# Kernel optimization log

Measured on AMD Instinct MI355X. Metric: run time of the kernel, lower is better.

Reference implementation:

```python
import jax, jax.numpy as jnp
import numpy as np

DIM = 1024
HEADS = 16
HEAD_DIM = DIM // HEADS
SCALE = HEAD_DIM ** -0.5
HIDDEN = 4 * DIM
EPS = 1e-5


def _ln(x, g, b):
    m = jnp.mean(x, -1, keepdims=True)
    v = jnp.mean(jnp.square(x - m), -1, keepdims=True)
    return (x - m) / jnp.sqrt(v + EPS) * g + b


def _attn(x, wqkv, qb, vb, wp, bp):
    # x: (B, N, C). qkv bias = concat(q_bias, zeros, v_bias) as in the torch code.
    B, N, C = x.shape
    bias = jnp.concatenate([qb, jnp.zeros_like(vb), vb])
    qkv = (x @ wqkv.T + bias).reshape(B, N, 3, HEADS, HEAD_DIM).transpose(2, 0, 3, 1, 4)
    q, k, v = qkv[0], qkv[1], qkv[2]
    # qk_float=True: logits computed in float32
    logits = jnp.einsum('bhqd,bhkd->bhqk', (q * SCALE).astype(jnp.float32), k.astype(jnp.float32))
    a = jax.nn.softmax(logits, axis=-1).astype(x.dtype)
    o = jnp.einsum('bhqk,bhkd->bqhd', a, v).reshape(B, N, C)
    return o @ wp.T + bp


def setup_inputs() -> dict:
    key = jax.random.key(0)
    ks = jax.random.split(key, 16)
    s = 0.02
    d = {
        'x': jax.random.normal(ks[0], (4, 8, 196, DIM), jnp.float32),
        'cls_token': jax.random.normal(ks[1], (4, DIM), jnp.float32),
        # temporal branch
        'tln_g': jnp.ones((DIM,), jnp.float32), 'tln_b': jnp.zeros((DIM,), jnp.float32),
        't_wqkv': jax.random.normal(ks[2], (3 * DIM, DIM), jnp.float32) * s,
        't_qb': jax.random.normal(ks[3], (DIM,), jnp.float32) * s,
        't_vb': jax.random.normal(ks[4], (DIM,), jnp.float32) * s,
        't_wproj': jax.random.normal(ks[5], (DIM, DIM), jnp.float32) * s,
        't_bproj': jnp.zeros((DIM,), jnp.float32),
        't_fc_w': jax.random.normal(ks[6], (DIM, DIM), jnp.float32) * s,
        't_fc_b': jnp.zeros((DIM,), jnp.float32),
        # spatial branch
        'n1_g': jnp.ones((DIM,), jnp.float32), 'n1_b': jnp.zeros((DIM,), jnp.float32),
        's_wqkv': jax.random.normal(ks[7], (3 * DIM, DIM), jnp.float32) * s,
        's_qb': jax.random.normal(ks[8], (DIM,), jnp.float32) * s,
        's_vb': jax.random.normal(ks[9], (DIM,), jnp.float32) * s,
        's_wproj': jax.random.normal(ks[10], (DIM, DIM), jnp.float32) * s,
        's_bproj': jnp.zeros((DIM,), jnp.float32),
        # mlp
        'n2_g': jnp.ones((DIM,), jnp.float32), 'n2_b': jnp.zeros((DIM,), jnp.float32),
        'fc1_w': jax.random.normal(ks[11], (HIDDEN, DIM), jnp.float32) * s,
        'fc1_b': jnp.zeros((HIDDEN,), jnp.float32),
        'fc2_w': jax.random.normal(ks[12], (DIM, HIDDEN), jnp.float32) * s,
        'fc2_b': jnp.zeros((DIM,), jnp.float32),
    }
    return d


def reference(x, cls_token, tln_g, tln_b, t_wqkv, t_qb, t_vb, t_wproj, t_bproj,
              t_fc_w, t_fc_b, n1_g, n1_b, s_wqkv, s_qb, s_vb, s_wproj, s_bproj,
              n2_g, n2_b, fc1_w, fc1_b, fc2_w, fc2_b):
    B, T, N, C = x.shape
    # temporal attention: 'b t n m -> (b n) t m'
    xt = x.transpose(0, 2, 1, 3).reshape(B * N, T, C)
    xt = _attn(_ln(xt, tln_g, tln_b), t_wqkv, t_qb, t_vb, t_wproj, t_bproj)
    # '(b n) t m -> b (n t) m'
    xt = xt.reshape(B, N * T, C)
    xt = xt @ t_fc_w.T + t_fc_b
    xt = x.transpose(0, 2, 1, 3).reshape(B, N * T, C) + xt
    # spatial attention with cls token per frame
    init_cls = cls_token[:, None, :]                               # (B, 1, C)
    cls_rep = jnp.broadcast_to(init_cls, (B, T, C)).reshape(B * T, 1, C)
    xs = xt.reshape(B, N, T, C).transpose(0, 2, 1, 3).reshape(B * T, N, C)
    xs = jnp.concatenate([cls_rep, xs], axis=1)                    # (B*T, N+1, C)
    xs = _attn(_ln(xs, n1_g, n1_b), s_wqkv, s_qb, s_vb, s_wproj, s_bproj)
    cls_m = xs[:, 0, :].reshape(B, T, C).mean(axis=1, keepdims=True)  # (B, 1, C)
    xs = xs[:, 1:, :].reshape(B, T, N, C).transpose(0, 2, 1, 3).reshape(B, N * T, C)
    x2 = jnp.concatenate([init_cls, xt], axis=1) + jnp.concatenate([cls_m, xs], axis=1)
    # MLP (exact GELU, matching nn.GELU default)
    h = _ln(x2, n2_g, n2_b)
    h = jax.nn.gelu(h @ fc1_w.T + fc1_b, approximate=False) @ fc2_w.T + fc2_b
    x2 = x2 + h
    cls_out = x2[:, 0, :]
    xo = x2[:, 1:].reshape(B, N, T, C).transpose(0, 2, 1, 3)       # (B, T, N, C)
    return xo, cls_out
```

## Files before the change

kernel.cpp:

```cpp
#include <hip/hip_runtime.h>
#include <stdint.h>


#define SCALE 0.125f

typedef unsigned short u16;
typedef short bf16x8 __attribute__((ext_vector_type(8)));
typedef float f32x4 __attribute__((ext_vector_type(4)));

static constexpr int kNT    = 1568;
static constexpr int kRowsA = 6272;
static constexpr int kSeqS  = 197;
static constexpr int kRowsS = 6304;
static constexpr int kRowsC = 6276;
static constexpr size_t kXO = 6422528;

__device__ __forceinline__ float bf2f(u16 u) {
    union { unsigned int i; float f; } c; c.i = ((unsigned int)u) << 16; return c.f;
}
__device__ __forceinline__ u16 f2bf(float f) {
    union { float f; unsigned int i; } c; c.f = f;
    unsigned int r = c.i + 0x7FFFu + ((c.i >> 16) & 1u);
    return (u16)(r >> 16);
}

__device__ __forceinline__ void gll16(const void* g, void* l) {
    __builtin_amdgcn_global_load_lds((__attribute__((address_space(1))) void*)g,
                                     (__attribute__((address_space(3))) void*)l,
                                     16, 0, 0);
}

__global__ void convw_k(const float* __restrict__ in, u16* __restrict__ out, int n4) {
    const int stride = gridDim.x * blockDim.x;
    for (int i = blockIdx.x * blockDim.x + threadIdx.x; i < n4; i += stride) {
        float4 v = ((const float4*)in)[i];
        ushort4 o;
        o.x = f2bf(v.x); o.y = f2bf(v.y); o.z = f2bf(v.z); o.w = f2bf(v.w);
        ((ushort4*)out)[i] = o;
    }
}

__global__ void bias3_k(const float* __restrict__ qb, const float* __restrict__ vb,
                        float* __restrict__ dst) {
    const int i = blockIdx.x * 256 + threadIdx.x;
    if (i >= 3072) return;
    dst[i] = (i < 1024) ? qb[i] : (i < 2048) ? 0.0f : vb[i - 2048];
}

template<int MODE>
__global__ void ln_k(const float* __restrict__ src, const float* __restrict__ src2,
                     const float* __restrict__ g, const float* __restrict__ bt,
                     u16* __restrict__ out, int rows) {
    const int r = (blockIdx.x << 2) + (threadIdx.x >> 6);
    const int lane = threadIdx.x & 63;
    if (r >= rows) return;
    const float* srow;
    if constexpr (MODE == 0) {
        int b = r / kNT, rem = r - b * kNT, n = rem >> 3, t = rem & 7;
        srow = src + (((size_t)((b * 8 + t) * 196 + n)) << 10);
    } else if constexpr (MODE == 1) {
        int s2 = r / kSeqS, i = r - s2 * kSeqS, b = s2 >> 3, t = s2 & 7;
        srow = (i == 0) ? (src2 + ((size_t)b << 10))
                        : (src + (((size_t)(b * kNT + ((i - 1) << 3) + t)) << 10));
    } else {
        srow = src + ((size_t)r << 10);
    }
    float4 v[4]; float s = 0.f, ss = 0.f;
#pragma unroll
    for (int j = 0; j < 4; ++j) {
        v[j] = *(const float4*)&srow[((j << 6) + lane) << 2];
        s  += v[j].x + v[j].y + v[j].z + v[j].w;
        ss += v[j].x * v[j].x + v[j].y * v[j].y + v[j].z * v[j].z + v[j].w * v[j].w;
    }
#pragma unroll
    for (int off = 1; off < 64; off <<= 1) { s += __shfl_xor(s, off); ss += __shfl_xor(ss, off); }
    const float mean = s * (1.f / 1024.f);
    const float rstd = rsqrtf(ss * (1.f / 1024.f) - mean * mean + 1e-5f);
#pragma unroll
    for (int j = 0; j < 4; ++j) {
        const int c = ((j << 6) + lane) << 2;
        float4 gg = *(const float4*)&g[c];
        float4 bb = *(const float4*)&bt[c];
        ushort4 o;
        o.x = f2bf((v[j].x - mean) * rstd * gg.x + bb.x);
        o.y = f2bf((v[j].y - mean) * rstd * gg.y + bb.y);
        o.z = f2bf((v[j].z - mean) * rstd * gg.z + bb.z);
        o.w = f2bf((v[j].w - mean) * rstd * gg.w + bb.w);
        *(ushort4*)&out[((size_t)r << 10) + c] = o;
    }
}

template<int MODE>
__global__ __launch_bounds__(256, 2) void gemm_bt(
        const u16* __restrict__ A, const u16* __restrict__ W,
        const float* __restrict__ bias,
        u16* __restrict__ outB, float* __restrict__ outF,
        const float* __restrict__ resid, float* __restrict__ dout,
        int M, int N, int K) {
    __shared__ __align__(16) u16 As[2][8192];
    __shared__ __align__(16) u16 Bs[2][8192];
    const int tid  = threadIdx.x;
    const int lane = tid & 63, wave = tid >> 6;
    const int lo = lane & 15, hi = lane >> 4;
    const int wr = wave >> 1, wc = wave & 1;
    const int row0 = blockIdx.y << 7, col0 = blockIdx.x << 7;

    const u16* aP[4]; const u16* bP[4];
#pragma unroll
    for (int i = 0; i < 4; ++i) {
        const int c = (wave << 8) + (i << 6) + lane;
        const int row = c >> 3;
        const int jl = ((c & 7) ^ (row & 7)) << 3;
        int ar = row0 + row; if (ar > M - 1) ar = M - 1;
        int br = col0 + row; if (br > N - 1) br = N - 1;
        aP[i] = A + (size_t)ar * K + jl;
        bP[i] = W + (size_t)br * K + jl;
    }

    f32x4 acc[4][4] = {};
    const int nk = K >> 6;

#pragma unroll
    for (int i = 0; i < 4; ++i) {
        u16* dA = &As[0][(wave << 11) + (i << 9)];
        u16* dB = &Bs[0][(wave << 11) + (i << 9)];
        gll16(aP[i], dA);
        gll16(bP[i], dB);
    }
    __syncthreads();

    int cur = 0;
    for (int it = 0; it < nk; ++it) {
        const bool more = (it + 1) < nk;
        if (more) {
            const int k1 = (it + 1) << 6;
#pragma unroll
            for (int i = 0; i < 4; ++i) {
                u16* dA = &As[cur ^ 1][(wave << 11) + (i << 9)];
                u16* dB = &Bs[cur ^ 1][(wave << 11) + (i << 9)];
                gll16(aP[i] + k1, dA);
                gll16(bP[i] + k1, dB);
            }
        }
        bf16x8 af[4][2], bfr[4][2];
#pragma unroll
        for (int m = 0; m < 4; ++m) {
            const int row = (wr << 6) + (m << 4) + lo;
#pragma unroll
            for (int h = 0; h < 2; ++h)
                af[m][h] = *(const bf16x8*)&As[cur][(row << 6) + ((((h << 2) + hi) ^ (lo & 7)) << 3)];
        }
#pragma unroll
        for (int n = 0; n < 4; ++n) {
            const int row = (wc << 6) + (n << 4) + lo;
#pragma unroll
            for (int h = 0; h < 2; ++h)
                bfr[n][h] = *(const bf16x8*)&Bs[cur][(row << 6) + ((((h << 2) + hi) ^ (lo & 7)) << 3)];
        }
#pragma unroll
        for (int m = 0; m < 4; ++m)
#pragma unroll
            for (int n = 0; n < 4; ++n) {
                acc[m][n] = __builtin_amdgcn_mfma_f32_16x16x32_bf16(af[m][0], bfr[n][0], acc[m][n], 0, 0, 0);
                acc[m][n] = __builtin_amdgcn_mfma_f32_16x16x32_bf16(af[m][1], bfr[n][1], acc[m][n], 0, 0, 0);
            }
        if (more) {
            __syncthreads();
            cur ^= 1;
        }
    }

#pragma unroll
    for (int m = 0; m < 4; ++m) {
        const int rb = row0 + (wr << 6) + (m << 4) + (hi << 2);
#pragma unroll
        for (int n = 0; n < 4; ++n) {
            const int c = col0 + (wc << 6) + (n << 4) + lo;
            const float bc = bias[c];
#pragma unroll
            for (int j = 0; j < 4; ++j) {
                const int r = rb + j;
                if (r >= M) continue;
                float v = acc[m][n][j] + bc;
                if constexpr (MODE == 2) v = 0.5f * v * (1.0f + erff(v * 0.70710678f));
                if constexpr (MODE == 3) {
                    int b = r / 1568, rem = r - b * 1568, nn = rem >> 3, tt = rem & 7;
                    v += resid[(((size_t)((b * 8 + tt) * 196 + nn)) << 10) + c];
                }
                if constexpr (MODE == 0 || MODE == 2) {
                    outB[(size_t)r * N + c] = f2bf(v);
                } else if constexpr (MODE == 1 || MODE == 3) {
                    outF[(size_t)r * N + c] = v;
                } else {
                    v += resid[((size_t)r << 10) + c];
                    int b = r / 1569, i = r - b * 1569;
                    if (i == 0) dout[kXO + ((size_t)b << 10) + c] = v;
                    else {
                        int jj = i - 1, nn = jj >> 3, tt = jj & 7;
                        dout[(((size_t)((b * 8 + tt) * 196 + nn)) << 10) + c] = v;
                    }
                }
            }
        }
    }
}

__global__ void attn_a_k(const u16* __restrict__ qkv, u16* __restrict__ o) {
    __shared__ float lq[4][8][65], lk[4][8][65], lv[4][8][65];
    __shared__ float al[4][64];
    const int lane = threadIdx.x & 63, wave = threadIdx.x >> 6;
    const int p = (blockIdx.x << 2) + wave;
    const int s = p >> 4, h = p & 15;
    const u16* base = qkv + (size_t)s * 24576 + (h << 6);
    for (int u = lane; u < 1536; u += 64) {
        const int part = u >> 9, t = (u >> 6) & 7, d = u & 63;
        const float val = bf2f(base[(size_t)t * 3072 + (part << 10) + d]);
        if (part == 0) lq[wave][t][d] = val;
        else if (part == 1) lk[wave][t][d] = val;
        else lv[wave][t][d] = val;
    }
    __syncthreads();
    const int qi = lane >> 3, kj = lane & 7;
    float dot = 0.f;
#pragma unroll
    for (int d = 0; d < 64; ++d) dot += lq[wave][qi][d] * lk[wave][kj][d];
    dot *= SCALE;
    float m = dot;
    m = fmaxf(m, __shfl_xor(m, 1));
    m = fmaxf(m, __shfl_xor(m, 2));
    m = fmaxf(m, __shfl_xor(m, 4));
    const float e = expf(dot - m);
    float sm = e;
    sm += __shfl_xor(sm, 1);
    sm += __shfl_xor(sm, 2);
    sm += __shfl_xor(sm, 4);
    al[wave][lane] = e / sm;
    __syncthreads();
    u16* orow = o + (size_t)s * 8192 + (h << 6) + lane;
#pragma unroll
    for (int ii = 0; ii < 8; ++ii) {
        float accv = 0.f;
#pragma unroll
        for (int jj = 0; jj < 8; ++jj) accv += al[wave][(ii << 3) + jj] * lv[wave][jj][lane];
        orow[(size_t)ii * 1024] = f2bf(accv);
    }
}

__global__ __launch_bounds__(256, 2) void attn_s_mfma(const u16* __restrict__ qkv,
                                                      u16* __restrict__ o) {
    __shared__ __align__(16) u16 SM[29696];
    u16* __restrict__ Vt = SM;
    const int tid = threadIdx.x, lane = tid & 63, wave = tid >> 6;
    const int lo = lane & 15, hi = lane >> 4;
    u16* __restrict__ Pw = SM + 14848 + wave * 3712;
    const int s2 = blockIdx.x >> 4, h = blockIdx.x & 15;
    const u16* __restrict__ base = qkv + (size_t)s2 * (kSeqS * 3072) + (h << 6);

    for (int u = tid; u < 26 * 64; u += 256) {
        const int d = u & 63, k0 = (u >> 6) << 3;
        union { bf16x8 v; u16 e[8]; } pk;
#pragma unroll
        for (int i = 0; i < 8; ++i) {
            int kr = k0 + i; if (kr > 196) kr = 196;
            pk.e[i] = base[(size_t)kr * 3072 + 2048 + d];
        }
        *(bf16x8*)&Vt[d * 232 + k0] = pk.v;
    }
    for (int u = tid; u < 1024; u += 256)
        Vt[(u >> 4) * 232 + 208 + (u & 15)] = 0;
    for (int u = lane; u < 256; u += 64)
        Pw[(u >> 4) * 232 + 208 + (u & 15)] = 0;
    __syncthreads();

    for (int qt = wave; qt < 13; qt += 4) {
        int qr = qt * 16 + lo; if (qr > 196) qr = 196;
        const u16* qp = base + (size_t)qr * 3072;
        const bf16x8 aq0 = *(const bf16x8*)&qp[hi << 3];
        const bf16x8 aq1 = *(const bf16x8*)&qp[32 + (hi << 3)];

        f32x4 s[13];
#pragma unroll
        for (int kt = 0; kt < 13; ++kt) {
            int kr = kt * 16 + lo; if (kr > 196) kr = 196;
            const u16* kp = base + (size_t)kr * 3072 + 1024;
            const bf16x8 bk0 = *(const bf16x8*)&kp[hi << 3];
            const bf16x8 bk1 = *(const bf16x8*)&kp[32 + (hi << 3)];
            f32x4 acc = {};
            acc = __builtin_amdgcn_mfma_f32_16x16x32_bf16(aq0, bk0, acc, 0, 0, 0);
            acc = __builtin_amdgcn_mfma_f32_16x16x32_bf16(aq1, bk1, acc, 0, 0, 0);
            s[kt] = acc * SCALE;
        }
        if (lo > 4) s[12] = (f32x4){-1e30f, -1e30f, -1e30f, -1e30f};

        float inv[4];
#pragma unroll
        for (int j = 0; j < 4; ++j) {
            float m = s[0][j];
#pragma unroll
            for (int kt = 1; kt < 13; ++kt) m = fmaxf(m, s[kt][j]);
            m = fmaxf(m, __shfl_xor(m, 1));
            m = fmaxf(m, __shfl_xor(m, 2));
            m = fmaxf(m, __shfl_xor(m, 4));
            m = fmaxf(m, __shfl_xor(m, 8));
            float sum = 0.f;
#pragma unroll
            for (int kt = 0; kt < 13; ++kt) {
                const float e = __expf(s[kt][j] - m);
                s[kt][j] = e;
                sum += e;
            }
            sum += __shfl_xor(sum, 1);
            sum += __shfl_xor(sum, 2);
            sum += __shfl_xor(sum, 4);
            sum += __shfl_xor(sum, 8);
            inv[j] = 1.f / sum;
        }

#pragma unroll
        for (int kt = 0; kt < 13; ++kt)
#pragma unroll
            for (int j = 0; j < 4; ++j)
                Pw[((hi << 2) + j) * 232 + kt * 16 + lo] = f2bf(s[kt][j]);

        f32x4 o4[4] = {};
#pragma unroll
        for (int kc = 0; kc < 7; ++kc) {
            const bf16x8 pa = *(const bf16x8*)&Pw[lo * 232 + kc * 32 + (hi << 3)];
#pragma unroll
            for (int dt = 0; dt < 4; ++dt) {
                const bf16x8 vf = *(const bf16x8*)&Vt[(dt * 16 + lo) * 232 + kc * 32 + (hi << 3)];
                o4[dt] = __builtin_amdgcn_mfma_f32_16x16x32_bf16(pa, vf, o4[dt], 0, 0, 0);
            }
        }

#pragma unroll
        for (int j = 0; j < 4; ++j) {
            const int q = qt * 16 + (hi << 2) + j;
            if (q > 196) continue;
            u16* orow = o + (((size_t)(s2 * kSeqS + q)) << 10) + (h << 6);
#pragma unroll
            for (int dt = 0; dt < 4; ++dt)
                orow[dt * 16 + lo] = f2bf(o4[dt][j] * inv[j]);
        }
    }
}

__global__ void clsm_k(const float* __restrict__ xs, float* __restrict__ cm) {
    const int idx = blockIdx.x * 256 + threadIdx.x;
    if (idx >= 4096) return;
    const int b = idx >> 10, c = idx & 1023;
    float s = 0.f;
#pragma unroll
    for (int t = 0; t < 8; ++t) s += xs[(((size_t)(b * 8 + t)) * kSeqS) * 1024 + c];
    cm[idx] = s * 0.125f;
}

__global__ void build_x2_k(const float* __restrict__ xt, const float* __restrict__ xs,
                           const float* __restrict__ cls, const float* __restrict__ cm,
                           float* __restrict__ x2) {
    const int r = blockIdx.x;
    const int c = threadIdx.x << 2;
    const int b = r / 1569, i = r - b * 1569;
    const float* pa; const float* pb;
    if (i == 0) {
        pa = cls + ((size_t)b << 10) + c;
        pb = cm + ((size_t)b << 10) + c;
    } else {
        const int jj = i - 1, n = jj >> 3, t = jj & 7;
        pa = xt + (((size_t)(b * 1568 + jj)) << 10) + c;
        pb = xs + (((size_t)((b * 8 + t) * kSeqS + 1 + n)) << 10) + c;
    }
    const float4 va = *(const float4*)pa;
    const float4 vb = *(const float4*)pb;
    float4 vo;
    vo.x = va.x + vb.x; vo.y = va.y + vb.y; vo.z = va.z + vb.z; vo.w = va.w + vb.w;
    *(float4*)&x2[((size_t)r << 10) + c] = vo;
}

extern "C" void kernel_launch(void* const* d_in, const int* in_sizes, int n_in,
                              void* d_out, int out_size, void* d_ws, size_t ws_size,
                              hipStream_t stream) {
    const float* x       = (const float*)d_in[0];
    const float* cls     = (const float*)d_in[1];
    const float* tln_g   = (const float*)d_in[2];
    const float* tln_b   = (const float*)d_in[3];
    const float* t_wqkv  = (const float*)d_in[4];
    const float* t_qb    = (const float*)d_in[5];
    const float* t_vb    = (const float*)d_in[6];
    const float* t_wproj = (const float*)d_in[7];
    const float* t_bproj = (const float*)d_in[8];
    const float* t_fc_w  = (const float*)d_in[9];
    const float* t_fc_b  = (const float*)d_in[10];
    const float* n1_g    = (const float*)d_in[11];
    const float* n1_b    = (const float*)d_in[12];
    const float* s_wqkv  = (const float*)d_in[13];
    const float* s_qb    = (const float*)d_in[14];
    const float* s_vb    = (const float*)d_in[15];
    const float* s_wproj = (const float*)d_in[16];
    const float* s_bproj = (const float*)d_in[17];
    const float* n2_g    = (const float*)d_in[18];
    const float* n2_b    = (const float*)d_in[19];
    const float* fc1_w   = (const float*)d_in[20];
    const float* fc1_b   = (const float*)d_in[21];
    const float* fc2_w   = (const float*)d_in[22];
    const float* fc2_b   = (const float*)d_in[23];
    float* dout = (float*)d_out;
    char* ws = (char*)d_ws;

    size_t off = 0;
    auto alloc = [&](size_t bytes) { size_t o = off; off += (bytes + 255) & ~(size_t)255; return o; };

    u16* t_wqkv_bf  = (u16*)(ws + alloc(3145728ull * 2));
    u16* t_wproj_bf = (u16*)(ws + alloc(1048576ull * 2));
    u16* t_fcw_bf   = (u16*)(ws + alloc(1048576ull * 2));
    u16* s_wqkv_bf  = (u16*)(ws + alloc(3145728ull * 2));
    u16* s_wproj_bf = (u16*)(ws + alloc(1048576ull * 2));
    u16* fc1_bf     = (u16*)(ws + alloc(4194304ull * 2));
    u16* fc2_bf     = (u16*)(ws + alloc(4194304ull * 2));
    u16* ln_bf      = (u16*)(ws + alloc((size_t)kRowsS * 1024 * 2));
    u16* qkv_bf     = (u16*)(ws + alloc((size_t)kRowsS * 3072 * 2));
    u16* o_bf       = (u16*)(ws + alloc((size_t)kRowsS * 1024 * 2));
    u16* h1_bf      = qkv_bf;
    u16* mid_bf     = (u16*)(ws + alloc((size_t)kRowsA * 1024 * 2));
    float* xt_f     = (float*)(ws + alloc((size_t)kRowsA * 1024 * 4));
    float* xs_f     = (float*)(ws + alloc((size_t)kRowsS * 1024 * 4));
    float* x2_f     = (float*)(ws + alloc((size_t)kRowsC * 1024 * 4));
    float* bias_t   = (float*)(ws + alloc(3072 * 4));
    float* bias_s   = (float*)(ws + alloc(3072 * 4));
    float* clsm     = (float*)(ws + alloc(4096 * 4));
    (void)ws_size; (void)in_sizes; (void)n_in; (void)out_size;

    convw_k<<<dim3(1024), dim3(256), 0, stream>>>(t_wqkv, t_wqkv_bf, 786432);
    convw_k<<<dim3(512),  dim3(256), 0, stream>>>(t_wproj, t_wproj_bf, 262144);
    convw_k<<<dim3(512),  dim3(256), 0, stream>>>(t_fc_w, t_fcw_bf, 262144);
    convw_k<<<dim3(1024), dim3(256), 0, stream>>>(s_wqkv, s_wqkv_bf, 786432);
    convw_k<<<dim3(512),  dim3(256), 0, stream>>>(s_wproj, s_wproj_bf, 262144);
    convw_k<<<dim3(1024), dim3(256), 0, stream>>>(fc1_w, fc1_bf, 1048576);
    convw_k<<<dim3(1024), dim3(256), 0, stream>>>(fc2_w, fc2_bf, 1048576);
    bias3_k<<<dim3(12), dim3(256), 0, stream>>>(t_qb, t_vb, bias_t);
    bias3_k<<<dim3(12), dim3(256), 0, stream>>>(s_qb, s_vb, bias_s);

    ln_k<0><<<dim3(kRowsA / 4), dim3(256), 0, stream>>>(x, nullptr, tln_g, tln_b, ln_bf, kRowsA);
    gemm_bt<0><<<dim3(24, 49), dim3(256), 0, stream>>>(ln_bf, t_wqkv_bf, bias_t, qkv_bf, nullptr, nullptr, nullptr, kRowsA, 3072, 1024);
    attn_a_k<<<dim3(3136), dim3(256), 0, stream>>>(qkv_bf, o_bf);
    gemm_bt<0><<<dim3(8, 49), dim3(256), 0, stream>>>(o_bf, t_wproj_bf, t_bproj, mid_bf, nullptr, nullptr, nullptr, kRowsA, 1024, 1024);
    gemm_bt<3><<<dim3(8, 49), dim3(256), 0, stream>>>(mid_bf, t_fcw_bf, t_fc_b, nullptr, xt_f, x, nullptr, kRowsA, 1024, 1024);

    ln_k<1><<<dim3(kRowsS / 4), dim3(256), 0, stream>>>(xt_f, cls, n1_g, n1_b, ln_bf, kRowsS);
    gemm_bt<0><<<dim3(24, 50), dim3(256), 0, stream>>>(ln_bf, s_wqkv_bf, bias_s, qkv_bf, nullptr, nullptr, nullptr, kRowsS, 3072, 1024);
    attn_s_mfma<<<dim3(512), dim3(256), 0, stream>>>(qkv_bf, o_bf);
    gemm_bt<1><<<dim3(8, 50), dim3(256), 0, stream>>>(o_bf, s_wproj_bf, s_bproj, nullptr, xs_f, nullptr, nullptr, kRowsS, 1024, 1024);
    clsm_k<<<dim3(16), dim3(256), 0, stream>>>(xs_f, clsm);
    build_x2_k<<<dim3(kRowsC), dim3(256), 0, stream>>>(xt_f, xs_f, cls, clsm, x2_f);

    ln_k<2><<<dim3(kRowsC / 4), dim3(256), 0, stream>>>(x2_f, nullptr, n2_g, n2_b, ln_bf, kRowsC);
    gemm_bt<2><<<dim3(32, 50), dim3(256), 0, stream>>>(ln_bf, fc1_bf, fc1_b, h1_bf, nullptr, nullptr, nullptr, kRowsC, 4096, 1024);
    gemm_bt<4><<<dim3(8, 50), dim3(256), 0, stream>>>(h1_bf, fc2_bf, fc2_b, nullptr, nullptr, x2_f, dout, kRowsC, 1024, 4096);
}
```

Baseline: 554.8 us.

## Template GEMM on M-tile size, halve K-step, use 64-row tiles for N=1024 GEMMs

```diff
diff --git a/kernel.cpp b/kernel.cpp
--- a/kernel.cpp
+++ b/kernel.cpp
@@ -90,80 +90,73 @@
     }
 }
 
-template<int MODE>
-__global__ __launch_bounds__(256, 2) void gemm_bt(
+template<int MODE, int TM>
+__global__ __launch_bounds__(256, 4) void gemm_bt(
         const u16* __restrict__ A, const u16* __restrict__ W,
         const float* __restrict__ bias,
         u16* __restrict__ outB, float* __restrict__ outF,
         const float* __restrict__ resid, float* __restrict__ dout,
         int M, int N, int K) {
-    __shared__ __align__(16) u16 As[2][8192];
-    __shared__ __align__(16) u16 Bs[2][8192];
+    constexpr int MF  = TM / 32;
+    constexpr int NCA = TM / 64;
+    __shared__ __align__(16) u16 As[2][TM * 32];
+    __shared__ __align__(16) u16 Bs[2][128 * 32];
     const int tid  = threadIdx.x;
     const int lane = tid & 63, wave = tid >> 6;
     const int lo = lane & 15, hi = lane >> 4;
     const int wr = wave >> 1, wc = wave & 1;
-    const int row0 = blockIdx.y << 7, col0 = blockIdx.x << 7;
-
-    const u16* aP[4]; const u16* bP[4];
-#pragma unroll
-    for (int i = 0; i < 4; ++i) {
-        const int c = (wave << 8) + (i << 6) + lane;
-        const int row = c >> 3;
-        const int jl = ((c & 7) ^ (row & 7)) << 3;
+    const int row0 = blockIdx.y * TM, col0 = blockIdx.x << 7;
+
+    const u16* aP[NCA]; const u16* bP[2];
+#pragma unroll
+    for (int i = 0; i < NCA; ++i) {
+        const int c = wave * TM + (i << 6) + lane;
+        const int row = c >> 2;
+        const int jl = (((c & 3) ^ (row & 3)) << 3);
         int ar = row0 + row; if (ar > M - 1) ar = M - 1;
+        aP[i] = A + (size_t)ar * K + jl;
+    }
+#pragma unroll
+    for (int i = 0; i < 2; ++i) {
+        const int c = (wave << 7) + (i << 6) + lane;
+        const int row = c >> 2;
+        const int jl = (((c & 3) ^ (row & 3)) << 3);
         int br = col0 + row; if (br > N - 1) br = N - 1;
-        aP[i] = A + (size_t)ar * K + jl;
         bP[i] = W + (size_t)br * K + jl;
     }
 
-    f32x4 acc[4][4] = {};
-    const int nk = K >> 6;
-
-#pragma unroll
-    for (int i = 0; i < 4; ++i) {
-        u16* dA = &As[0][(wave << 11) + (i << 9)];
-        u16* dB = &Bs[0][(wave << 11) + (i << 9)];
-        gll16(aP[i], dA);
-        gll16(bP[i], dB);
-    }
+    f32x4 acc[MF][4] = {};
+    const int nk = K >> 5;
+
+    auto stage = [&](int buf, int k0) {
+#pragma unroll
+        for (int i = 0; i < NCA; ++i)
+            gll16(aP[i] + k0, &As[buf][wave * (TM * 8) + (i << 9)]);
+#pragma unroll
+        for (int i = 0; i < 2; ++i)
+            gll16(bP[i] + k0, &Bs[buf][(wave << 10) + (i << 9)]);
+    };
+
+    stage(0, 0);
     __syncthreads();
 
     int cur = 0;
     for (int it = 0; it < nk; ++it) {
         const bool more = (it + 1) < nk;
-        if (more) {
-            const int k1 = (it + 1) << 6;
-#pragma unroll
-            for (int i = 0; i < 4; ++i) {
-                u16* dA = &As[cur ^ 1][(wave << 11) + (i << 9)];
-                u16* dB = &Bs[cur ^ 1][(wave << 11) + (i << 9)];
-                gll16(aP[i] + k1, dA);
-                gll16(bP[i] + k1, dB);
-            }
-        }
-        bf16x8 af[4][2], bfr[4][2];
-#pragma unroll
-        for (int m = 0; m < 4; ++m) {
-            const int row = (wr << 6) + (m << 4) + lo;
-#pragma unroll
-            for (int h = 0; h < 2; ++h)
-                af[m][h] = *(const bf16x8*)&As[cur][(row << 6) + ((((h << 2) + hi) ^ (lo & 7)) << 3)];
-        }
-#pragma unroll
-        for (int n = 0; n < 4; ++n) {
-            const int row = (wc << 6) + (n << 4) + lo;
-#pragma unroll
-            for (int h = 0; h < 2; ++h)
-                bfr[n][h] = *(const bf16x8*)&Bs[cur][(row << 6) + ((((h << 2) + hi) ^ (lo & 7)) << 3)];
-        }
-#pragma unroll
-        for (int m = 0; m < 4; ++m)
-#pragma unroll
-            for (int n = 0; n < 4; ++n) {
-                acc[m][n] = __builtin_amdgcn_mfma_f32_16x16x32_bf16(af[m][0], bfr[n][0], acc[m][n], 0, 0, 0);
-                acc[m][n] = __builtin_amdgcn_mfma_f32_16x16x32_bf16(af[m][1], bfr[n][1], acc[m][n], 0, 0, 0);
-            }
+        if (more) stage(cur ^ 1, (it + 1) << 5);
+        const int sl = (hi ^ (lo & 3)) << 3;
+        bf16x8 af[MF], bfr[4];
+#pragma unroll
+        for (int m = 0; m < MF; ++m)
+            af[m] = *(const bf16x8*)&As[cur][((wr * (TM / 2) + (m << 4) + lo) << 5) + sl];
+#pragma unroll
+        for (int n = 0; n < 4; ++n)
+            bfr[n] = *(const bf16x8*)&Bs[cur][(((wc << 6) + (n << 4) + lo) << 5) + sl];
+#pragma unroll
+        for (int m = 0; m < MF; ++m)
+#pragma unroll
+            for (int n = 0; n < 4; ++n)
+                acc[m][n] = __builtin_amdgcn_mfma_f32_16x16x32_bf16(af[m], bfr[n], acc[m][n], 0, 0, 0);
         if (more) {
             __syncthreads();
             cur ^= 1;
@@ -171,8 +164,8 @@
     }
 
 #pragma unroll
-    for (int m = 0; m < 4; ++m) {
-        const int rb = row0 + (wr << 6) + (m << 4) + (hi << 2);
+    for (int m = 0; m < MF; ++m) {
+        const int rb = row0 + wr * (TM / 2) + (m << 4) + (hi << 2);
 #pragma unroll
         for (int n = 0; n < 4; ++n) {
             const int c = col0 + (wc << 6) + (n << 4) + lo;
@@ -441,19 +434,19 @@
     bias3_k<<<dim3(12), dim3(256), 0, stream>>>(s_qb, s_vb, bias_s);
 
     ln_k<0><<<dim3(kRowsA / 4), dim3(256), 0, stream>>>(x, nullptr, tln_g, tln_b, ln_bf, kRowsA);
-    gemm_bt<0><<<dim3(24, 49), dim3(256), 0, stream>>>(ln_bf, t_wqkv_bf, bias_t, qkv_bf, nullptr, nullptr, nullptr, kRowsA, 3072, 1024);
+    gemm_bt<0, 128><<<dim3(24, 49), dim3(256), 0, stream>>>(ln_bf, t_wqkv_bf, bias_t, qkv_bf, nullptr, nullptr, nullptr, kRowsA, 3072, 1024);
     attn_a_k<<<dim3(3136), dim3(256), 0, stream>>>(qkv_bf, o_bf);
-    gemm_bt<0><<<dim3(8, 49), dim3(256), 0, stream>>>(o_bf, t_wproj_bf, t_bproj, mid_bf, nullptr, nullptr, nullptr, kRowsA, 1024, 1024);
-    gemm_bt<3><<<dim3(8, 49), dim3(256), 0, stream>>>(mid_bf, t_fcw_bf, t_fc_b, nullptr, xt_f, x, nullptr, kRowsA, 1024, 1024);
+    gemm_bt<0, 64><<<dim3(8, 98), dim3(256), 0, stream>>>(o_bf, t_wproj_bf, t_bproj, mid_bf, nullptr, nullptr, nullptr, kRowsA, 1024, 1024);
+    gemm_bt<3, 64><<<dim3(8, 98), dim3(256), 0, stream>>>(mid_bf, t_fcw_bf, t_fc_b, nullptr, xt_f, x, nullptr, kRowsA, 1024, 1024);
 
     ln_k<1><<<dim3(kRowsS / 4), dim3(256), 0, stream>>>(xt_f, cls, n1_g, n1_b, ln_bf, kRowsS);
-    gemm_bt<0><<<dim3(24, 50), dim3(256), 0, stream>>>(ln_bf, s_wqkv_bf, bias_s, qkv_bf, nullptr, nullptr, nullptr, kRowsS, 3072, 1024);
+    gemm_bt<0, 128><<<dim3(24, 50), dim3(256), 0, stream>>>(ln_bf, s_wqkv_bf, bias_s, qkv_bf, nullptr, nullptr, nullptr, kRowsS, 3072, 1024);
     attn_s_mfma<<<dim3(512), dim3(256), 0, stream>>>(qkv_bf, o_bf);
-    gemm_bt<1><<<dim3(8, 50), dim3(256), 0, stream>>>(o_bf, s_wproj_bf, s_bproj, nullptr, xs_f, nullptr, nullptr, kRowsS, 1024, 1024);
+    gemm_bt<1, 64><<<dim3(8, 99), dim3(256), 0, stream>>>(o_bf, s_wproj_bf, s_bproj, nullptr, xs_f, nullptr, nullptr, kRowsS, 1024, 1024);
     clsm_k<<<dim3(16), dim3(256), 0, stream>>>(xs_f, clsm);
     build_x2_k<<<dim3(kRowsC), dim3(256), 0, stream>>>(xt_f, xs_f, cls, clsm, x2_f);
 
     ln_k<2><<<dim3(kRowsC / 4), dim3(256), 0, stream>>>(x2_f, nullptr, n2_g, n2_b, ln_bf, kRowsC);
-    gemm_bt<2><<<dim3(32, 50), dim3(256), 0, stream>>>(ln_bf, fc1_bf, fc1_b, h1_bf, nullptr, nullptr, nullptr, kRowsC, 4096, 1024);
-    gemm_bt<4><<<dim3(8, 50), dim3(256), 0, stream>>>(h1_bf, fc2_bf, fc2_b, nullptr, nullptr, x2_f, dout, kRowsC, 1024, 4096);
-}
+    gemm_bt<2, 128><<<dim3(32, 50), dim3(256), 0, stream>>>(ln_bf, fc1_bf, fc1_b, h1_bf, nullptr, nullptr, nullptr, kRowsC, 4096, 1024);
+    gemm_bt<4, 64><<<dim3(8, 99), dim3(256), 0, stream>>>(h1_bf, fc2_bf, fc2_b, nullptr, nullptr, x2_f, dout, kRowsC, 1024, 4096);
+}
```

New measurement: 553.8 us. No clear change (-0.2%).
